# Kernel tuning notes

Measured on AMD Instinct MI355X. Metric: run time of the kernel, lower is better.

Reference implementation:

```python
import jax, jax.numpy as jnp
import numpy as np

HID = 4096
NH = 32
NKV = 8
HD = 128
KV_OUT = NKV * HD  # 1024
B, S = 1, 2048
SCALE = 64.0
THETA = 500000.0


def fwht(x):
    """Normalized fast Walsh-Hadamard transform over last dim (power of 2).
    Matches matmul_hadU_cuda for the had=None, K=1 case."""
    *lead, n = x.shape
    x = x.reshape(-1, n)
    h = 1
    while h < n:  # log2(n) static iterations
        x = x.reshape(-1, n // (2 * h), 2, h)
        a, b = x[:, :, 0, :], x[:, :, 1, :]
        x = jnp.stack([a + b, a - b], axis=2).reshape(-1, n)
        h *= 2
    return (x * (1.0 / np.sqrt(n))).reshape(*lead, n)


def rope_cos_sin(position_ids, dim=HD, theta=THETA):
    inv_freq = 1.0 / (theta ** (jnp.arange(0, dim, 2, dtype=jnp.float32) / dim))
    freqs = position_ids.astype(jnp.float32)[..., None] * inv_freq  # [B,S,HD/2]
    emb = jnp.concatenate([freqs, freqs], axis=-1)  # [B,S,HD]
    return jnp.cos(emb), jnp.sin(emb)


def rotate_half(x):
    h = x.shape[-1] // 2
    return jnp.concatenate([-x[..., h:], x[..., :h]], axis=-1)


def setup_inputs() -> dict:
    key = jax.random.key(0)
    ks = jax.random.split(key, 10)
    return {
        "hidden_states": jax.random.normal(ks[0], (B, S, HID), jnp.float32),
        "position_ids": jnp.arange(S, dtype=jnp.int32)[None, :],
        "SU_qkv": jnp.sign(jax.random.normal(ks[1], (HID,), jnp.float32)),
        "SU_o": jnp.sign(jax.random.normal(ks[2], (HID,), jnp.float32)),
        "Wscale_qkv": jax.random.uniform(ks[3], (HID + 2 * KV_OUT,), jnp.float32, 0.5, 1.5),
        "Wscale_o": jax.random.uniform(ks[4], (HID,), jnp.float32, 0.5, 1.5),
        "Wq": 0.02 * jax.random.normal(ks[5], (HID, HID), jnp.float32),
        "Wk": 0.02 * jax.random.normal(ks[6], (KV_OUT, HID), jnp.float32),
        "Wv": 0.02 * jax.random.normal(ks[7], (KV_OUT, HID), jnp.float32),
        "Wo": 0.02 * jax.random.normal(ks[8], (HID, HID), jnp.float32),
    }


def reference(hidden_states, position_ids, SU_qkv, SU_o, Wscale_qkv, Wscale_o, Wq, Wk, Wv, Wo):
    b, s, n = hidden_states.shape
    # --- compute_qkv: incoherence rotation + quantized-linear math ---
    x = fwht(hidden_states * SU_qkv) / SCALE  # [B,S,HID]
    q = (x @ Wq.T) * Wscale_qkv[:HID] * SCALE
    k = (x @ Wk.T) * Wscale_qkv[HID:HID + KV_OUT] * SCALE
    v = (x @ Wv.T) * Wscale_qkv[HID + KV_OUT:] * SCALE
    q = q.reshape(b, s, NH, HD).transpose(0, 2, 1, 3)   # [B,NH,S,HD]
    k = k.reshape(b, s, NKV, HD).transpose(0, 2, 1, 3)  # [B,NKV,S,HD]
    v = v.reshape(b, s, NKV, HD).transpose(0, 2, 1, 3)
    # --- RoPE ---
    cos, sin = rope_cos_sin(position_ids)
    cos, sin = cos[:, None], sin[:, None]  # [B,1,S,HD]
    q = q * cos + rotate_half(q) * sin
    k = k * cos + rotate_half(k) * sin
    # --- GQA repeat + causal SDPA ---
    rep = NH // NKV
    k = jnp.repeat(k, rep, axis=1)
    v = jnp.repeat(v, rep, axis=1)
    scores = jnp.einsum('bhqd,bhkd->bhqk', q, k) / np.sqrt(HD)
    causal = jnp.tril(jnp.ones((s, s), dtype=bool))
    scores = jnp.where(causal, scores, -1e30)
    attn = jax.nn.softmax(scores, axis=-1)
    out = jnp.einsum('bhqk,bhkd->bhqd', attn, v)
    out = out.transpose(0, 2, 1, 3).reshape(b, s, NH * HD)  # [B,S,HID]
    # --- compute_o ---
    y = fwht(out * SU_o) / SCALE
    y = (y @ Wo.T) * Wscale_o * SCALE
    return y
```

## Files before the change

kernel.cpp:

```cpp
#include <hip/hip_runtime.h>
#include <hip/hip_bf16.h>
#include <math.h>

#define S_LEN 2048
#define HID   4096
#define NQKV  6144
#define NHEAD 32
#define NKVH  8
#define HDIM  128

typedef __attribute__((ext_vector_type(8))) short short8;
typedef __attribute__((ext_vector_type(4))) float f32x4;

__device__ __forceinline__ unsigned short f2bf(float f) {
    union { float f; unsigned u; } v; v.f = f;
    unsigned r = v.u + 0x7fffu + ((v.u >> 16) & 1u);
    return (unsigned short)(r >> 16);
}
__device__ __forceinline__ float bf2f(unsigned short b) {
    union { unsigned u; float f; } v; v.u = ((unsigned)b) << 16;
    return v.f;
}
__device__ __forceinline__ unsigned cvt_pk_bf16(float lo, float hi) {
    unsigned r;
    asm("v_cvt_pk_bf16_f32 %0, %1, %2" : "=v"(r) : "v"(lo), "v"(hi));
    return r;
}

__device__ __forceinline__ void fwht_lds_radix4(float* buf) {
    int lg = 0;
    for (int h = 1; h < HID; h <<= 2, lg += 2) {
        for (int p = threadIdx.x; p < HID / 4; p += 256) {
            int j  = p & (h - 1);
            int i0 = ((p >> lg) << (lg + 2)) | j;
            float a = buf[i0], b = buf[i0 + h], c = buf[i0 + 2 * h], d = buf[i0 + 3 * h];
            float apb = a + b, amb = a - b, cpd = c + d, cmd = c - d;
            buf[i0]         = apb + cpd;
            buf[i0 + h]     = amb + cmd;
            buf[i0 + 2 * h] = apb - cpd;
            buf[i0 + 3 * h] = amb - cmd;
        }
        __syncthreads();
    }
}

__global__ __launch_bounds__(256)
void cvt4_kernel(const float* __restrict__ Wq, const float* __restrict__ Wk,
                 const float* __restrict__ Wv, const float* __restrict__ Wo,
                 unsigned short* __restrict__ Wcat, unsigned short* __restrict__ Wob) {
    const int NQ = 4194304, NK = 1048576, NV = 1048576, NO = 4194304;
    int i = blockIdx.x * 256 + threadIdx.x;
    const int stride = gridDim.x * 256;
    for (; i < NQ + NK + NV + NO; i += stride) {
        const float* src; unsigned short* dst; int j;
        if (i < NQ)                { src = Wq; dst = Wcat;            j = i; }
        else if (i < NQ + NK)      { src = Wk; dst = Wcat + 16777216; j = i - NQ; }
        else if (i < NQ + NK + NV) { src = Wv; dst = Wcat + 20971520; j = i - NQ - NK; }
        else                       { src = Wo; dst = Wob;             j = i - NQ - NK - NV; }
        float4 v = *(const float4*)(src + (size_t)j * 4);
        ushort4 o;
        o.x = f2bf(v.x); o.y = f2bf(v.y); o.z = f2bf(v.z); o.w = f2bf(v.w);
        *(ushort4*)(dst + (size_t)j * 4) = o;
    }
}

__global__ __launch_bounds__(256)
void fwht_kernel(const float* __restrict__ in, const float* __restrict__ su,
                 unsigned short* __restrict__ out) {
    __shared__ float buf[HID];
    const float* src = in + (size_t)blockIdx.x * HID;
    for (int i = threadIdx.x; i < HID; i += 256) buf[i] = src[i] * su[i];
    __syncthreads();
    fwht_lds_radix4(buf);
    unsigned short* dst = out + (size_t)blockIdx.x * HID;
    const float norm = 1.0f / 4096.0f;
    for (int i = threadIdx.x; i < HID; i += 256) dst[i] = f2bf(buf[i] * norm);
}

__global__ __launch_bounds__(256)
void fwht_merge(const unsigned short* __restrict__ O1, const float* __restrict__ ML,
                const float* __restrict__ su, unsigned short* __restrict__ out) {
    __shared__ float buf[HID];
    __shared__ float w1s[NHEAD], w2s[NHEAD];
    const int q = blockIdx.x;
    if (threadIdx.x < NHEAD) {
        const float2* mlp = (const float2*)ML;
        float2 a = mlp[((size_t)q) * NHEAD + threadIdx.x];
        float2 b = mlp[((size_t)(S_LEN + q)) * NHEAD + threadIdx.x];
        float M = fmaxf(a.x, b.x);
        float e1 = exp2f(a.x - M), e2 = exp2f(b.x - M);
        float L = e1 * a.y + e2 * b.y;
        w1s[threadIdx.x] = e1 / L;
        w2s[threadIdx.x] = e2 / L;
    }
    __syncthreads();
    const unsigned short* r1 = O1 + (size_t)q * HID;
    const unsigned short* r2 = O1 + (size_t)(S_LEN + q) * HID;
    for (int i = threadIdx.x; i < HID; i += 256) {
        int hd = i >> 7;
        buf[i] = (bf2f(r1[i]) * w1s[hd] + bf2f(r2[i]) * w2s[hd]) * su[i];
    }
    __syncthreads();
    fwht_lds_radix4(buf);
    unsigned short* dst = out + (size_t)q * HID;
    const float norm = 1.0f / 4096.0f;
    for (int i = threadIdx.x; i < HID; i += 256) dst[i] = f2bf(buf[i] * norm);
}

__global__ __launch_bounds__(256)
void gemm_bt(const unsigned short* __restrict__ A, const unsigned short* __restrict__ B,
             const float* __restrict__ scale, float* __restrict__ C,
             int M, int N, int K) {
    __shared__ __attribute__((aligned(16))) unsigned short As[2][128 * 32];
    __shared__ __attribute__((aligned(16))) unsigned short Bs[2][128 * 32];
    const int bn = blockIdx.x, bm = blockIdx.y;
    const int tid = threadIdx.x;
    const int wv = tid >> 6, lane = tid & 63;
    const int wr = wv >> 1, wc = wv & 1;
    const int lr = lane & 15, lgp = lane >> 4;

    f32x4 acc[4][4] = {};

    auto stage = [&](int buf, int kt) {
        for (int c = wv; c < 8; c += 4) {
            int o = c * 512 + lane * 8;
            int row = o >> 5, col = o & 31;
            const unsigned short* ga = A + (size_t)(bm * 128 + row) * K + kt * 32 + col;
            __builtin_amdgcn_global_load_lds((const __attribute__((address_space(1))) void*)ga,
                (__attribute__((address_space(3))) void*)&As[buf][c * 512], 16, 0, 0);
            const unsigned short* gb = B + (size_t)(bn * 128 + row) * K + kt * 32 + col;
            __builtin_amdgcn_global_load_lds((const __attribute__((address_space(1))) void*)gb,
                (__attribute__((address_space(3))) void*)&Bs[buf][c * 512], 16, 0, 0);
        }
    };

    const int nt = K >> 5;
    stage(0, 0);
    __syncthreads();
    int cur = 0;
    for (int kt = 0; kt < nt; ++kt) {
        if (kt + 1 < nt) stage(cur ^ 1, kt + 1);
        const int ko = lgp * 8;
        short8 af[4], bfr[4];
#pragma unroll
        for (int m2 = 0; m2 < 4; ++m2)
            af[m2] = *(const short8*)&As[cur][(wr * 64 + m2 * 16 + lr) * 32 + ko];
#pragma unroll
        for (int n2 = 0; n2 < 4; ++n2)
            bfr[n2] = *(const short8*)&Bs[cur][(wc * 64 + n2 * 16 + lr) * 32 + ko];
#pragma unroll
        for (int m2 = 0; m2 < 4; ++m2)
#pragma unroll
            for (int n2 = 0; n2 < 4; ++n2)
                acc[m2][n2] = __builtin_amdgcn_mfma_f32_16x16x32_bf16(af[m2], bfr[n2], acc[m2][n2], 0, 0, 0);
        __syncthreads();
        cur ^= 1;
    }

#pragma unroll
    for (int n2 = 0; n2 < 4; ++n2) {
        int gn = bn * 128 + wc * 64 + n2 * 16 + lr;
        float sc = scale[gn] * 64.0f;
#pragma unroll
        for (int m2 = 0; m2 < 4; ++m2) {
            int gm0 = bm * 128 + wr * 64 + m2 * 16 + lgp * 4;
#pragma unroll
            for (int i = 0; i < 4; ++i)
                C[(size_t)(gm0 + i) * N + gn] = acc[m2][n2][i] * sc;
        }
    }
}

__global__ __launch_bounds__(256)
void gemm_qkv(const unsigned short* __restrict__ A, const unsigned short* __restrict__ B,
              const float* __restrict__ scale, const int* __restrict__ pos,
              unsigned short* __restrict__ Qb, unsigned short* __restrict__ Kb,
              unsigned short* __restrict__ Vb) {
    const int K = HID;
    __shared__ __attribute__((aligned(16))) unsigned short As[2][128 * 32];
    __shared__ __attribute__((aligned(16))) unsigned short Bs[2][128 * 32];
    __shared__ float invf_t[64];
    __shared__ float poss[128];
    const int bn = blockIdx.x, bm = blockIdx.y;
    const int tid = threadIdx.x;
    const int wv = tid >> 6, lane = tid & 63;
    const int wr = wv >> 1, wc = wv & 1;
    const int lr = lane & 15, lgp = lane >> 4;

    if (tid < 64) invf_t[tid] = exp2f((float)tid * -0.29580576f);
    if (tid >= 128) poss[tid - 128] = (float)pos[bm * 128 + (tid - 128)];

    f32x4 acc[4][4] = {};

    auto stage = [&](int buf, int kt) {
        for (int c = wv; c < 8; c += 4) {
            int o = c * 512 + lane * 8;
            int row = o >> 5, col = o & 31;
            const unsigned short* ga = A + (size_t)(bm * 128 + row) * K + kt * 32 + col;
            __builtin_amdgcn_global_load_lds((const __attribute__((address_space(1))) void*)ga,
                (__attribute__((address_space(3))) void*)&As[buf][c * 512], 16, 0, 0);
            int prow = (row & 31) | ((row & 32) << 1) | ((row & 64) >> 1);
            const unsigned short* gb = B + (size_t)(bn * 128 + prow) * K + kt * 32 + col;
            __builtin_amdgcn_global_load_lds((const __attribute__((address_space(1))) void*)gb,
                (__attribute__((address_space(3))) void*)&Bs[buf][c * 512], 16, 0, 0);
        }
    };

    const int nt = K >> 5;
    stage(0, 0);
    __syncthreads();
    int cur = 0;
    for (int kt = 0; kt < nt; ++kt) {
        if (kt + 1 < nt) stage(cur ^ 1, kt + 1);
        const int ko = lgp * 8;
        short8 af[4], bfr[4];
#pragma unroll
        for (int m2 = 0; m2 < 4; ++m2)
            af[m2] = *(const short8*)&As[cur][(wr * 64 + m2 * 16 + lr) * 32 + ko];
#pragma unroll
        for (int n2 = 0; n2 < 4; ++n2)
            bfr[n2] = *(const short8*)&Bs[cur][(wc * 64 + n2 * 16 + lr) * 32 + ko];
#pragma unroll
        for (int m2 = 0; m2 < 4; ++m2)
#pragma unroll
            for (int n2 = 0; n2 < 4; ++n2)
                acc[m2][n2] = __builtin_amdgcn_mfma_f32_16x16x32_bf16(af[m2], bfr[n2], acc[m2][n2], 0, 0, 0);
        __syncthreads();
        cur ^= 1;
    }

    const int nb = bn * 128;
    const float QS = 0.12751793f;
#pragma unroll
    for (int n2 = 0; n2 < 2; ++n2) {
        const int d = n2 * 16 + lr + wc * 32;
        const float sc_lo = scale[nb + d] * 64.0f;
        const float sc_hi = scale[nb + d + 64] * 64.0f;
        const float ivf = invf_t[d];
#pragma unroll
        for (int m2 = 0; m2 < 4; ++m2) {
#pragma unroll
            for (int i = 0; i < 4; ++i) {
                const int lrow = wr * 64 + m2 * 16 + lgp * 4 + i;
                const int srow = bm * 128 + lrow;
                float lo = acc[m2][n2][i] * sc_lo;
                float hi = acc[m2][n2 + 2][i] * sc_hi;
                float olo, ohi;
                if (bn < 40) {
                    float sn, cs;
                    sincosf(poss[lrow] * ivf, &sn, &cs);
                    olo = lo * cs - hi * sn;
                    ohi = hi * cs + lo * sn;
                } else { olo = lo; ohi = hi; }
                unsigned short* dst;
                if (bn < 32)      { dst = Qb + ((size_t)bn * S_LEN + srow) * HDIM; olo *= QS; ohi *= QS; }
                else if (bn < 40) { dst = Kb + ((size_t)(bn - 32) * S_LEN + srow) * HDIM; }
                else              { dst = Vb + ((size_t)(bn - 40) * S_LEN + srow) * HDIM; }
                dst[d]      = f2bf(olo);
                dst[d + 64] = f2bf(ohi);
            }
        }
    }
}

__global__ __launch_bounds__(256)
void attn_kernel(const unsigned short* __restrict__ Q, const unsigned short* __restrict__ K,
                 const unsigned short* __restrict__ V, unsigned short* __restrict__ Opart,
                 float* __restrict__ ML) {
    const int hf = blockIdx.y;
    const int hd = blockIdx.z;
    const int kvh = hd >> 2;
    const int tid = threadIdx.x, wv = tid >> 6, lane = tid & 63;
    const int lr = lane & 15, lgp = lane >> 4;

    __shared__ __attribute__((aligned(16))) unsigned short Ks[2][64 * 128];
    __shared__ __attribute__((aligned(16))) unsigned short Vt[128 * 64];

    int koff[4];
#pragma unroll
    for (int j = 0; j < 4; ++j) {
        int a = (wv * 4 + j) * 512 + lane * 8;
        koff[j] = a ^ (((a >> 7) & 7) << 3);
    }
    const int vpos = ((lane >> 2) & 3) * 16 + (lane >> 4) * 4 + (lane & 3);
    const unsigned short* Kg = K + (size_t)kvh * S_LEN * HDIM;
    const unsigned short* Vg = V + (size_t)kvh * S_LEN * HDIM;

    auto stageK = [&](int buf, int kb) {
        const unsigned short* kg = Kg + (size_t)kb * 64 * HDIM;
#pragma unroll
        for (int j = 0; j < 4; ++j) {
            __builtin_amdgcn_global_load_lds(
                (const __attribute__((address_space(1))) void*)(kg + koff[j]),
                (__attribute__((address_space(3))) void*)&Ks[buf][(wv * 4 + j) * 512], 16, 0, 0);
        }
    };

#pragma unroll 1
    for (int rep = 0; rep < 2; ++rep) {
        const int qt = rep ? (31 - (int)blockIdx.x) : (int)blockIdx.x;
        const int qg = qt * 64 + wv * 16 + lr;
        const int n = qt + 1, mid = (n + 1) >> 1;
        const int s = hf ? mid : 0, e = hf ? n : mid;

        __syncthreads();

        short8 aq[4];
        {
            const unsigned short* qp = Q + ((size_t)hd * S_LEN + qg) * HDIM + lgp * 8;
#pragma unroll
            for (int kk = 0; kk < 4; ++kk) aq[kk] = *(const short8*)(qp + kk * 32);
        }

        f32x4 oacc[8] = {};
        float m_i = -3.0e38f, l_i = 0.f;

        short8 vcur[4];
        if (s < e) {
            stageK(s & 1, s);
            const unsigned short* vp = Vg + (size_t)s * 64 * HDIM + lane * HDIM + wv * 32;
#pragma unroll
            for (int r2 = 0; r2 < 4; ++r2) vcur[r2] = *(const short8*)(vp + r2 * 8);
        }

#pragma unroll 1
        for (int kb = s; kb < e; ++kb) {
            const int cur = kb & 1;
            __syncthreads();

            if (kb + 1 < e) stageK(cur ^ 1, kb + 1);
#pragma unroll
            for (int r2 = 0; r2 < 4; ++r2) {
#pragma unroll
                for (int en = 0; en < 8; ++en) {
                    int d = wv * 32 + r2 * 8 + en;
                    Vt[(d * 64 + vpos) ^ ((d & 7) << 3)] = ((const unsigned short*)&vcur[r2])[en];
                }
            }
            if (kb + 1 < e) {
                const unsigned short* vp = Vg + (size_t)(kb + 1) * 64 * HDIM + lane * HDIM + wv * 32;
#pragma unroll
                for (int r2 = 0; r2 < 4; ++r2) vcur[r2] = *(const short8*)(vp + r2 * 8);
            }

            __builtin_amdgcn_s_setprio(1);
            f32x4 sc[4];
#pragma unroll
            for (int nt2 = 0; nt2 < 4; ++nt2) {
                f32x4 a = {};
                const int krow = nt2 * 16 + lr;
                const int swz = (krow & 7) << 3;
#pragma unroll
                for (int kk = 0; kk < 4; ++kk) {
                    short8 ak = *(const short8*)&Ks[cur][(krow * 128 + kk * 32 + lgp * 8) ^ swz];
                    a = __builtin_amdgcn_mfma_f32_16x16x32_bf16(ak, aq[kk], a, 0, 0, 0);
                }
                sc[nt2] = a;
            }
            __builtin_amdgcn_s_setprio(0);

            if (kb == qt) {
#pragma unroll
                for (int nt2 = 0; nt2 < 4; ++nt2)
#pragma unroll
                    for (int i = 0; i < 4; ++i) {
                        int kvg = kb * 64 + nt2 * 16 + 4 * lgp + i;
                        if (kvg > qg) sc[nt2][i] = -1.0e30f;
                    }
            }

            float vmax = fmaxf(fmaxf(fmaxf(sc[0][0], sc[0][1]), fmaxf(sc[0][2], sc[0][3])),
                               fmaxf(fmaxf(sc[1][0], sc[1][1]), fmaxf(sc[1][2], sc[1][3])));
            vmax = fmaxf(vmax, fmaxf(fmaxf(fmaxf(sc[2][0], sc[2][1]), fmaxf(sc[2][2], sc[2][3])),
                                     fmaxf(fmaxf(sc[3][0], sc[3][1]), fmaxf(sc[3][2], sc[3][3]))));
            vmax = fmaxf(vmax, __shfl_xor(vmax, 16));
            vmax = fmaxf(vmax, __shfl_xor(vmax, 32));

            if (!__all(vmax <= m_i + 11.0f)) {
                float mn = fmaxf(m_i, vmax);
                float fe = __builtin_amdgcn_exp2f(m_i - mn);
                m_i = mn;
                l_i *= fe;
                float feb[4];
#pragma unroll
                for (int i2 = 0; i2 < 4; ++i2) feb[i2] = __shfl(fe, 4 * lgp + i2);
#pragma unroll
                for (int t = 0; t < 8; ++t)
#pragma unroll
                    for (int i2 = 0; i2 < 4; ++i2) oacc[t][i2] *= feb[i2];
            }

            float rs = 0.f;
#pragma unroll
            for (int nt2 = 0; nt2 < 4; ++nt2)
#pragma unroll
                for (int i = 0; i < 4; ++i) {
                    float pv = __builtin_amdgcn_exp2f(sc[nt2][i] - m_i);
                    sc[nt2][i] = pv;
                    rs += pv;
                }
            rs += __shfl_xor(rs, 16);
            rs += __shfl_xor(rs, 32);
            l_i += rs;

            union { unsigned u[4]; short8 sv; } a0, a1;
            a0.u[0] = cvt_pk_bf16(sc[0][0], sc[0][1]);
            a0.u[1] = cvt_pk_bf16(sc[0][2], sc[0][3]);
            a0.u[2] = cvt_pk_bf16(sc[1][0], sc[1][1]);
            a0.u[3] = cvt_pk_bf16(sc[1][2], sc[1][3]);
            a1.u[0] = cvt_pk_bf16(sc[2][0], sc[2][1]);
            a1.u[1] = cvt_pk_bf16(sc[2][2], sc[2][3]);
            a1.u[2] = cvt_pk_bf16(sc[3][0], sc[3][1]);
            a1.u[3] = cvt_pk_bf16(sc[3][2], sc[3][3]);

            asm volatile("s_waitcnt lgkmcnt(0)" ::: "memory");
            __builtin_amdgcn_sched_barrier(0);
            __builtin_amdgcn_s_barrier();

            __builtin_amdgcn_s_setprio(1);
#pragma unroll
            for (int t = 0; t < 8; ++t) {
                const int d = t * 16 + lr;
                const int swz = (d & 7) << 3;
                const int dbase = d * 64 + lgp * 16;
                short8 bv0 = *(const short8*)&Vt[(dbase) ^ swz];
                short8 bv1 = *(const short8*)&Vt[(dbase + 8) ^ swz];
                oacc[t] = __builtin_amdgcn_mfma_f32_16x16x32_bf16(a0.sv, bv0, oacc[t], 0, 0, 0);
                oacc[t] = __builtin_amdgcn_mfma_f32_16x16x32_bf16(a1.sv, bv1, oacc[t], 0, 0, 0);
            }
            __builtin_amdgcn_s_setprio(0);
        }

        unsigned short* op = Opart + ((size_t)hf * S_LEN + qt * 64 + wv * 16 + 4 * lgp) * HID
                           + hd * HDIM + lr;
#pragma unroll
        for (int t = 0; t < 8; ++t)
#pragma unroll
            for (int i2 = 0; i2 < 4; ++i2)
                op[(size_t)i2 * HID + t * 16] = f2bf(oacc[t][i2]);
        if (lgp == 0) {
            float2* mlp = (float2*)ML;
            mlp[((size_t)hf * S_LEN + qt * 64 + wv * 16 + lr) * NHEAD + hd] =
                make_float2(m_i, l_i);
        }
    }
}

extern "C" void kernel_launch(void* const* d_in, const int* in_sizes, int n_in,
                              void* d_out, int out_size, void* d_ws, size_t ws_size,
                              hipStream_t stream) {
    const float* hidden = (const float*)d_in[0];
    const int*   pos    = (const int*)d_in[1];
    const float* su_qkv = (const float*)d_in[2];
    const float* su_o   = (const float*)d_in[3];
    const float* ws_qkv = (const float*)d_in[4];
    const float* ws_o   = (const float*)d_in[5];
    const float* Wq     = (const float*)d_in[6];
    const float* Wk     = (const float*)d_in[7];
    const float* Wv     = (const float*)d_in[8];
    const float* Wo     = (const float*)d_in[9];
    float* out = (float*)d_out;

    char* ws = (char*)d_ws;
    unsigned short* Wcat = (unsigned short*)(ws);
    unsigned short* Wob  = (unsigned short*)(ws + 50331648);
    unsigned short* xb   = (unsigned short*)(ws + 83886080);
    unsigned short* Opart= (unsigned short*)(ws + 100663296);
    float*          ML   = (float*)(ws + 100663296 + 33554432);
    unsigned short* Qb   = (unsigned short*)(ws + 150994944);
    unsigned short* Kb   = Qb + (size_t)NHEAD * S_LEN * HDIM;
    unsigned short* Vb   = Kb + (size_t)NKVH * S_LEN * HDIM;

    cvt4_kernel<<<2560, 256, 0, stream>>>(Wq, Wk, Wv, Wo, Wcat, Wob);

    fwht_kernel<<<S_LEN, 256, 0, stream>>>(hidden, su_qkv, xb);
    gemm_qkv<<<dim3(NQKV / 128, S_LEN / 128), 256, 0, stream>>>(xb, Wcat, ws_qkv, pos, Qb, Kb, Vb);
    attn_kernel<<<dim3(16, 2, NHEAD), 256, 0, stream>>>(Qb, Kb, Vb, Opart, ML);
    fwht_merge<<<S_LEN, 256, 0, stream>>>(Opart, ML, su_o, xb);
    gemm_bt<<<dim3(HID / 128, S_LEN / 128), 256, 0, stream>>>(xb, Wob, ws_o, out, S_LEN, HID, HID);
}
```

Baseline: 409.9 us.

## Merge prep kernels, fold output scales into bf16 weights, precompute RoPE table

Combines the weight conversion and the input FWHT into one prep launch, which also builds a cos/sin RoPE table. The per-row Wscale*64 factors (and the Q softmax scale) are folded into the bf16 weights during conversion, so the GEMM epilogues no longer apply scales or call sincosf. This saves a kernel launch and the epilogue transcendental work. In exchange, rounding happens after scaling, so numerics shift slightly, and the GEMM epilogue gains extra global reads for the RoPE table.

Result: slower. 472.7 us (+15.3%).

```diff
diff --git a/kernel.cpp b/kernel.cpp
--- a/kernel.cpp
+++ b/kernel.cpp
@@ -45,36 +45,58 @@
 }
 
 __global__ __launch_bounds__(256)
-void cvt4_kernel(const float* __restrict__ Wq, const float* __restrict__ Wk,
+void prep_kernel(const float* __restrict__ hidden, const float* __restrict__ su,
+                 const int* __restrict__ pos,
+                 const float* __restrict__ ws_qkv, const float* __restrict__ ws_o,
+                 const float* __restrict__ Wq, const float* __restrict__ Wk,
                  const float* __restrict__ Wv, const float* __restrict__ Wo,
-                 unsigned short* __restrict__ Wcat, unsigned short* __restrict__ Wob) {
-    const int NQ = 4194304, NK = 1048576, NV = 1048576, NO = 4194304;
-    int i = blockIdx.x * 256 + threadIdx.x;
-    const int stride = gridDim.x * 256;
-    for (; i < NQ + NK + NV + NO; i += stride) {
-        const float* src; unsigned short* dst; int j;
-        if (i < NQ)                { src = Wq; dst = Wcat;            j = i; }
-        else if (i < NQ + NK)      { src = Wk; dst = Wcat + 16777216; j = i - NQ; }
-        else if (i < NQ + NK + NV) { src = Wv; dst = Wcat + 20971520; j = i - NQ - NK; }
-        else                       { src = Wo; dst = Wob;             j = i - NQ - NK - NV; }
-        float4 v = *(const float4*)(src + (size_t)j * 4);
-        ushort4 o;
-        o.x = f2bf(v.x); o.y = f2bf(v.y); o.z = f2bf(v.z); o.w = f2bf(v.w);
-        *(ushort4*)(dst + (size_t)j * 4) = o;
-    }
-}
-
-__global__ __launch_bounds__(256)
-void fwht_kernel(const float* __restrict__ in, const float* __restrict__ su,
-                 unsigned short* __restrict__ out) {
+                 unsigned short* __restrict__ xb, unsigned short* __restrict__ Wcat,
+                 unsigned short* __restrict__ Wob, float2* __restrict__ ropetab) {
     __shared__ float buf[HID];
-    const float* src = in + (size_t)blockIdx.x * HID;
-    for (int i = threadIdx.x; i < HID; i += 256) buf[i] = src[i] * su[i];
-    __syncthreads();
-    fwht_lds_radix4(buf);
-    unsigned short* dst = out + (size_t)blockIdx.x * HID;
-    const float norm = 1.0f / 4096.0f;
-    for (int i = threadIdx.x; i < HID; i += 256) dst[i] = f2bf(buf[i] * norm);
+    int b = blockIdx.x;
+    if (b < S_LEN) {
+        const float* src = hidden + (size_t)b * HID;
+        for (int i = threadIdx.x; i < HID; i += 256) buf[i] = src[i] * su[i];
+        __syncthreads();
+        fwht_lds_radix4(buf);
+        unsigned short* dst = xb + (size_t)b * HID;
+        const float norm = 1.0f / 4096.0f;
+        for (int i = threadIdx.x; i < HID; i += 256) dst[i] = f2bf(buf[i] * norm);
+        return;
+    }
+    b -= S_LEN;
+    if (b < 2560) {
+        const int NQ = 4194304, NK = 1048576, NV = 1048576, NO = 4194304;
+        const float QS = 0.12751793f;
+        int i = b * 256 + threadIdx.x;
+        const int stride = 2560 * 256;
+        for (; i < NQ + NK + NV + NO; i += stride) {
+            const float* src; unsigned short* dst; int j; float sc;
+            if (i < NQ)                { src = Wq; dst = Wcat;            j = i;
+                                         sc = ws_qkv[j >> 10] * 64.0f * QS; }
+            else if (i < NQ + NK)      { src = Wk; dst = Wcat + 16777216; j = i - NQ;
+                                         sc = ws_qkv[4096 + (j >> 10)] * 64.0f; }
+            else if (i < NQ + NK + NV) { src = Wv; dst = Wcat + 20971520; j = i - NQ - NK;
+                                         sc = ws_qkv[5120 + (j >> 10)] * 64.0f; }
+            else                       { src = Wo; dst = Wob;             j = i - NQ - NK - NV;
+                                         sc = ws_o[j >> 10] * 64.0f; }
+            float4 v = *(const float4*)(src + (size_t)j * 4);
+            ushort4 o;
+            o.x = f2bf(v.x * sc); o.y = f2bf(v.y * sc);
+            o.z = f2bf(v.z * sc); o.w = f2bf(v.w * sc);
+            *(ushort4*)(dst + (size_t)j * 4) = o;
+        }
+        return;
+    }
+    b -= 2560;
+    for (int it = 0; it < 32; ++it) {
+        int t = b * 8192 + it * 256 + threadIdx.x;
+        int s = t >> 6, j = t & 63;
+        float ang = (float)pos[s] * exp2f((float)j * -0.29580576f);
+        float sn, cs;
+        sincosf(ang, &sn, &cs);
+        ropetab[t] = make_float2(cs, sn);
+    }
 }
 
 __global__ __launch_bounds__(256)
@@ -109,8 +131,7 @@
 
 __global__ __launch_bounds__(256)
 void gemm_bt(const unsigned short* __restrict__ A, const unsigned short* __restrict__ B,
-             const float* __restrict__ scale, float* __restrict__ C,
-             int M, int N, int K) {
+             float* __restrict__ C, int M, int N, int K) {
     __shared__ __attribute__((aligned(16))) unsigned short As[2][128 * 32];
     __shared__ __attribute__((aligned(16))) unsigned short Bs[2][128 * 32];
     const int bn = blockIdx.x, bm = blockIdx.y;
@@ -160,35 +181,29 @@
 #pragma unroll
     for (int n2 = 0; n2 < 4; ++n2) {
         int gn = bn * 128 + wc * 64 + n2 * 16 + lr;
-        float sc = scale[gn] * 64.0f;
 #pragma unroll
         for (int m2 = 0; m2 < 4; ++m2) {
             int gm0 = bm * 128 + wr * 64 + m2 * 16 + lgp * 4;
 #pragma unroll
             for (int i = 0; i < 4; ++i)
-                C[(size_t)(gm0 + i) * N + gn] = acc[m2][n2][i] * sc;
+                C[(size_t)(gm0 + i) * N + gn] = acc[m2][n2][i];
         }
     }
 }
 
 __global__ __launch_bounds__(256)
 void gemm_qkv(const unsigned short* __restrict__ A, const unsigned short* __restrict__ B,
-              const float* __restrict__ scale, const int* __restrict__ pos,
+              const float2* __restrict__ ropetab,
               unsigned short* __restrict__ Qb, unsigned short* __restrict__ Kb,
               unsigned short* __restrict__ Vb) {
     const int K = HID;
     __shared__ __attribute__((aligned(16))) unsigned short As[2][128 * 32];
     __shared__ __attribute__((aligned(16))) unsigned short Bs[2][128 * 32];
-    __shared__ float invf_t[64];
-    __shared__ float poss[128];
     const int bn = blockIdx.x, bm = blockIdx.y;
     const int tid = threadIdx.x;
     const int wv = tid >> 6, lane = tid & 63;
     const int wr = wv >> 1, wc = wv & 1;
     const int lr = lane & 15, lgp = lane >> 4;
-
-    if (tid < 64) invf_t[tid] = exp2f((float)tid * -0.29580576f);
-    if (tid >= 128) poss[tid - 128] = (float)pos[bm * 128 + (tid - 128)];
 
     f32x4 acc[4][4] = {};
 
@@ -229,33 +244,27 @@
         cur ^= 1;
     }
 
-    const int nb = bn * 128;
-    const float QS = 0.12751793f;
 #pragma unroll
     for (int n2 = 0; n2 < 2; ++n2) {
         const int d = n2 * 16 + lr + wc * 32;
-        const float sc_lo = scale[nb + d] * 64.0f;
-        const float sc_hi = scale[nb + d + 64] * 64.0f;
-        const float ivf = invf_t[d];
 #pragma unroll
         for (int m2 = 0; m2 < 4; ++m2) {
 #pragma unroll
             for (int i = 0; i < 4; ++i) {
                 const int lrow = wr * 64 + m2 * 16 + lgp * 4 + i;
                 const int srow = bm * 128 + lrow;
-                float lo = acc[m2][n2][i] * sc_lo;
-                float hi = acc[m2][n2 + 2][i] * sc_hi;
+                float lo = acc[m2][n2][i];
+                float hi = acc[m2][n2 + 2][i];
                 float olo, ohi;
                 if (bn < 40) {
-                    float sn, cs;
-                    sincosf(poss[lrow] * ivf, &sn, &cs);
-                    olo = lo * cs - hi * sn;
-                    ohi = hi * cs + lo * sn;
+                    float2 t = ropetab[(size_t)srow * 64 + d];
+                    olo = lo * t.x - hi * t.y;
+                    ohi = hi * t.x + lo * t.y;
                 } else { olo = lo; ohi = hi; }
                 unsigned short* dst;
-                if (bn < 32)      { dst = Qb + ((size_t)bn * S_LEN + srow) * HDIM; olo *= QS; ohi *= QS; }
-                else if (bn < 40) { dst = Kb + ((size_t)(bn - 32) * S_LEN + srow) * HDIM; }
-                else              { dst = Vb + ((size_t)(bn - 40) * S_LEN + srow) * HDIM; }
+                if (bn < 32)      dst = Qb + ((size_t)bn * S_LEN + srow) * HDIM;
+                else if (bn < 40) dst = Kb + ((size_t)(bn - 32) * S_LEN + srow) * HDIM;
+                else              dst = Vb + ((size_t)(bn - 40) * S_LEN + srow) * HDIM;
                 dst[d]      = f2bf(olo);
                 dst[d + 64] = f2bf(ohi);
             }
@@ -466,16 +475,16 @@
     unsigned short* Wob  = (unsigned short*)(ws + 50331648);
     unsigned short* xb   = (unsigned short*)(ws + 83886080);
     unsigned short* Opart= (unsigned short*)(ws + 100663296);
-    float*          ML   = (float*)(ws + 100663296 + 33554432);
+    float*          ML   = (float*)(ws + 134217728);
+    float2*         rtab = (float2*)(ws + 136314880);
     unsigned short* Qb   = (unsigned short*)(ws + 150994944);
     unsigned short* Kb   = Qb + (size_t)NHEAD * S_LEN * HDIM;
     unsigned short* Vb   = Kb + (size_t)NKVH * S_LEN * HDIM;
 
-    cvt4_kernel<<<2560, 256, 0, stream>>>(Wq, Wk, Wv, Wo, Wcat, Wob);
-
-    fwht_kernel<<<S_LEN, 256, 0, stream>>>(hidden, su_qkv, xb);
-    gemm_qkv<<<dim3(NQKV / 128, S_LEN / 128), 256, 0, stream>>>(xb, Wcat, ws_qkv, pos, Qb, Kb, Vb);
+    prep_kernel<<<4624, 256, 0, stream>>>(hidden, su_qkv, pos, ws_qkv, ws_o,
+                                          Wq, Wk, Wv, Wo, xb, Wcat, Wob, rtab);
+    gemm_qkv<<<dim3(NQKV / 128, S_LEN / 128), 256, 0, stream>>>(xb, Wcat, rtab, Qb, Kb, Vb);
     attn_kernel<<<dim3(16, 2, NHEAD), 256, 0, stream>>>(Qb, Kb, Vb, Opart, ML);
     fwht_merge<<<S_LEN, 256, 0, stream>>>(Opart, ML, su_o, xb);
-    gemm_bt<<<dim3(HID / 128, S_LEN / 128), 256, 0, stream>>>(xb, Wob, ws_o, out, S_LEN, HID, HID);
-}
+    gemm_bt<<<dim3(HID / 128, S_LEN / 128), 256, 0, stream>>>(xb, Wob, out, S_LEN, HID, HID);
+}
```
